# Kernel tuning notes

Hardware: AMD Instinct MI355X
Metric: run time of the kernel (lower is better)

The kernel has to match this reference:

```python
import jax, jax.numpy as jnp
import numpy as np
from jax import lax

C = 16  # channels

def _conv1x1(x, w, b):
    # 1x1x1 Conv3d == channel-mixing einsum. x: [B,C,T,H,W], w: [O,C], b: [O]
    return jnp.einsum('oc,bcthw->bothw', w, x) + b[None, :, None, None, None]

def _ffn(x, w1, b1, w2, b2):
    return _conv1x1(jnp.tanh(_conv1x1(x, w1, b1)), w2, b2)

def setup_inputs() -> dict:
    key = jax.random.key(0)
    ks = jax.random.split(key, 12)
    s = 0.1
    x = jax.random.normal(ks[0], (2, C, 31, 256, 256), dtype=jnp.float32)
    mk_w = lambda k: jax.random.normal(k, (C, C), dtype=jnp.float32) * s
    mk_b = lambda k: jax.random.normal(k, (C,), dtype=jnp.float32) * s
    return {
        'x': x,
        'wf1': mk_w(ks[1]), 'bf1': mk_b(ks[2]),
        'wf2': mk_w(ks[3]), 'bf2': mk_b(ks[4]),
        'ww1': mk_w(ks[5]), 'bw1': mk_b(ks[6]),
        'ww2': mk_w(ks[7]), 'bw2': mk_b(ks[8]),
        'wsca': mk_w(ks[9]), 'bsca': mk_b(ks[10]),
    }

def reference(x, wf1, bf1, wf2, bf2, ww1, bw1, ww2, bw2, wsca, bsca):
    # Gates from two 1x1-conv FFNs
    Z = jnp.tanh(_ffn(x, wf1, bf1, wf2, bf2))          # [B,C,T,H,W]
    Fg = jax.nn.sigmoid(_ffn(x, ww1, bw1, ww2, bw2))   # [B,C,T,H,W]
    # Linear recurrence over time dim: h_t = f_t * h_{t-1} + (1-f_t) * z_t, h_{-1}=0
    Zt = jnp.moveaxis(Z, 2, 0)   # [T,B,C,H,W]
    Ft = jnp.moveaxis(Fg, 2, 0)
    def step(h, zf):
        z, f = zf
        h = f * h + (1.0 - f) * z
        return h, h
    h0 = jnp.zeros_like(Zt[0])
    _, hs = lax.scan(step, h0, (Zt, Ft))
    out = jnp.moveaxis(hs, 0, 2)  # [B,C,T,H,W]
    # Simplified channel attention: global avg pool -> 1x1 conv -> sigmoid -> scale
    gap = jnp.mean(out, axis=(2, 3, 4), keepdims=True)  # [B,C,1,1,1]
    att = jax.nn.sigmoid(_conv1x1(gap, wsca, bsca))
    return att * out
```

## Files before the change

kernel.cpp:

```cpp
#include <hip/hip_runtime.h>
#include <hip/hip_bf16.h>

#define TDIM 31
#define TS   65536
#define CS   (TDIM * TS)
#define BS   (16 * CS)
#define NTOT (2 * BS)
#define K1_BLOCKS 8192
#define GAP_INV (1.0f / (31.0f * 65536.0f))

typedef __attribute__((ext_vector_type(8))) short short8v;
typedef __attribute__((ext_vector_type(4))) float f32x4;
typedef __attribute__((ext_vector_type(8))) unsigned short ushort8v;

__device__ __forceinline__ float frcp(float v){ return __builtin_amdgcn_rcpf(v); }
__device__ __forceinline__ float fexp2_(float v){ return __builtin_amdgcn_exp2f(v); }
__device__ __forceinline__ float ftanh(float x){ float e = fexp2_(x*2.8853900817779268f); return 1.0f - 2.0f*frcp(e+1.0f); }
__device__ __forceinline__ float fsigm(float x){ float e = fexp2_(x*-1.4426950408889634f); return frcp(1.0f+e); }
__device__ __forceinline__ unsigned rhu16(float x){ return (__float_as_uint(x) + 0x8000u) >> 16; }
__device__ __forceinline__ float bf2f(unsigned b){ return __uint_as_float(b << 16); }
__device__ __forceinline__ unsigned pkhi(unsigned u0, unsigned u1){ return __builtin_amdgcn_perm(u1, u0, 0x07060302u); }

template<bool BF16H>
__global__ __launch_bounds__(256, 4) void k1_fused(
    const float* __restrict__ x,
    const float* __restrict__ wf1, const float* __restrict__ bf1,
    const float* __restrict__ wf2, const float* __restrict__ bf2,
    const float* __restrict__ ww1, const float* __restrict__ bw1,
    const float* __restrict__ ww2, const float* __restrict__ bw2,
    float* __restrict__ out, unsigned short* __restrict__ hb,
    float* __restrict__ partials)
{
    __shared__ unsigned int sGate[TDIM * 256];

    const int tid  = threadIdx.x;
    const int lane = tid & 63;
    const int wv   = tid >> 6;
    const int col  = lane & 15;
    const int kg   = lane >> 4;
    const bool lok = (kg >= 2);
    const int blk  = blockIdx.x;
    const int b    = blk >> 12;
    const int p0   = (blk & 4095) << 4;

    short8v A1f, A2f, A1w, A2w, Af2, Aw2;
    {
        const int c0 = (kg & 1) * 8;
#pragma unroll
        for (int i = 0; i < 8; ++i) {
            const float w1 = wf1[col*16 + c0 + i];
            unsigned u1 = __float_as_uint(w1);
            float lo1 = w1 - __uint_as_float(u1 & 0xFFFF0000u);
            A1f[i] = (short)(u1 >> 16);
            A2f[i] = (short)(__float_as_uint(lo1) >> 16);
            const float w2 = ww1[col*16 + c0 + i];
            unsigned u2 = __float_as_uint(w2);
            float lo2 = w2 - __uint_as_float(u2 & 0xFFFF0000u);
            A1w[i] = (short)(u2 >> 16);
            A2w[i] = (short)(__float_as_uint(lo2) >> 16);
            const float v2f = wf2[col*16 + c0 + i];
            const float v2w = ww2[col*16 + c0 + i];
            Af2[i] = (kg < 2)  ? (short)rhu16(v2f) : (short)0;
            Aw2[i] = (kg >= 2) ? (short)rhu16(v2w) : (short)0;
        }
    }
    f32x4 b1fv, b1wv, b2fv, b2wv;
#pragma unroll
    for (int r = 0; r < 4; ++r) {
        b1fv[r] = bf1[kg*4+r]; b1wv[r] = bw1[kg*4+r];
        b2fv[r] = bf2[kg*4+r]; b2wv[r] = bw2[kg*4+r];
    }

    const int lsrc = col + ((kg & 1) << 5);

    auto process = [&](int u, const float* xv) {
        unsigned H[4], L[4];
#pragma unroll
        for (int j = 0; j < 4; ++j) {
            const unsigned u0 = __float_as_uint(xv[2*j]);
            const unsigned u1 = __float_as_uint(xv[2*j+1]);
            const float l0 = xv[2*j]   - __uint_as_float(u0 & 0xFFFF0000u);
            const float l1 = xv[2*j+1] - __uint_as_float(u1 & 0xFFFF0000u);
            H[j] = pkhi(u0, u1);
            L[j] = pkhi(__float_as_uint(l0), __float_as_uint(l1));
        }
        uint4 bxu;
        bxu.x = lok ? L[0] : H[0]; bxu.y = lok ? L[1] : H[1];
        bxu.z = lok ? L[2] : H[2]; bxu.w = lok ? L[3] : H[3];
        const short8v bx = __builtin_bit_cast(short8v, bxu);

        f32x4 accf = b1fv, accw = b1wv;
        accf = __builtin_amdgcn_mfma_f32_16x16x32_bf16(A1f, bx, accf, 0, 0, 0);
        accf = __builtin_amdgcn_mfma_f32_16x16x32_bf16(A2f, bx, accf, 0, 0, 0);
        accw = __builtin_amdgcn_mfma_f32_16x16x32_bf16(A1w, bx, accw, 0, 0, 0);
        accw = __builtin_amdgcn_mfma_f32_16x16x32_bf16(A2w, bx, accw, 0, 0, 0);

        const float a0 = ftanh(accf[0]), a1 = ftanh(accf[1]);
        const float a2 = ftanh(accf[2]), a3 = ftanh(accf[3]);
        const float w0 = ftanh(accw[0]), w1 = ftanh(accw[1]);
        const float w2 = ftanh(accw[2]), w3 = ftanh(accw[3]);
        const unsigned afP0 = (rhu16(a1) << 16) | rhu16(a0);
        const unsigned afP1 = (rhu16(a3) << 16) | rhu16(a2);
        const unsigned awP0 = (rhu16(w1) << 16) | rhu16(w0);
        const unsigned awP1 = (rhu16(w3) << 16) | rhu16(w2);

        const unsigned x0l = __shfl(afP0, lsrc, 64);
        const unsigned x1l = __shfl(afP1, lsrc, 64);
        const unsigned x0h = __shfl(afP0, lsrc + 16, 64);
        const unsigned x1h = __shfl(afP1, lsrc + 16, 64);
        const unsigned y0l = __shfl(awP0, lsrc, 64);
        const unsigned y1l = __shfl(awP1, lsrc, 64);
        const unsigned y0h = __shfl(awP0, lsrc + 16, 64);
        const unsigned y1h = __shfl(awP1, lsrc + 16, 64);
        uint4 b2u;
        b2u.x = lok ? y0l : x0l;
        b2u.y = lok ? y1l : x1l;
        b2u.z = lok ? y0h : x0h;
        b2u.w = lok ? y1h : x1h;
        const short8v b2 = __builtin_bit_cast(short8v, b2u);

        f32x4 acz = b2fv, acw = b2wv;
        acz = __builtin_amdgcn_mfma_f32_16x16x32_bf16(Af2, b2, acz, 0, 0, 0);
        acw = __builtin_amdgcn_mfma_f32_16x16x32_bf16(Aw2, b2, acw, 0, 0, 0);

#pragma unroll
        for (int r = 0; r < 4; ++r) {
            const float z = ftanh(acz[r]);
            const float f = fsigm(acw[r]);
            const int   zi = (int)__builtin_rintf(z * 32767.0f);
            const unsigned fu = (unsigned)(f * 65535.0f + 0.5f);
            const unsigned wd = ((unsigned)zi << 16) | (fu & 0xFFFFu);
            sGate[u*256 + r*64 + (kg>>1)*32 + (((r ^ kg) & 1) << 4)
                  + ((col + 4*r) & 15)] = wd;
        }
    };

    const unsigned xbase = (unsigned)b * BS + (unsigned)p0 + (unsigned)col
                         + (unsigned)((kg & 1) * 8) * CS;
#define LOADU(dst, u_) { const float* xp = x + (size_t)xbase + (size_t)(u_) * TS; \
    _Pragma("unroll") for (int i = 0; i < 8; ++i) (dst)[i] = xp[i * CS]; }

    float xs0[8], xs1[8], xs2[8], xs3[8];
    LOADU(xs0, wv)
    LOADU(xs1, wv + 4)
    LOADU(xs2, wv + 8)
#pragma unroll
    for (int k = 0; k < 8; ++k) {
        const int u  = wv + 4 * k;
        const int uf = u + 12;
        switch (k & 3) {
            case 0: if (uf < TDIM) LOADU(xs3, uf) if (u < TDIM) process(u, xs0); break;
            case 1: if (uf < TDIM) LOADU(xs0, uf) if (u < TDIM) process(u, xs1); break;
            case 2: if (uf < TDIM) LOADU(xs1, uf) if (u < TDIM) process(u, xs2); break;
            default:if (uf < TDIM) LOADU(xs2, uf) if (u < TDIM) process(u, xs3); break;
        }
    }
#undef LOADU
    __syncthreads();

    {
        const int c = tid >> 4, p = tid & 15;
        const unsigned base2 = (unsigned)((c & 3) * 64 + ((c >> 3) & 1) * 32
                             + (((c ^ (c >> 2)) & 1) << 4) + ((p + 4 * c) & 15));
        const unsigned obase = (unsigned)b * BS + (unsigned)c * CS
                             + (unsigned)p0 + (unsigned)p;
        float h = 0.f, s = 0.f;
#pragma unroll 1
        for (int t = 0; t < TDIM; ++t) {
            const unsigned wd = sGate[t * 256 + base2];
            const float z = (float)((int)wd >> 16) * (1.0f / 32767.0f);
            const float f = (float)(wd & 0xFFFFu) * (1.0f / 65535.0f);
            h = fmaf(f, h - z, z);
            s += h;
            if (BF16H) hb[obase + (unsigned)t * TS] = (unsigned short)rhu16(h);
            else       out[obase + (unsigned)t * TS] = h;
        }
#pragma unroll
        for (int off = 8; off; off >>= 1) s += __shfl_down(s, off, 16);
        if (p == 0) partials[blk * 16 + c] = s;
    }
}

__global__ __launch_bounds__(1024) void k2_attention(
    const float* __restrict__ partials, const float* __restrict__ wsca,
    const float* __restrict__ bsca, float* __restrict__ att)
{
    __shared__ float red[2][16][32];
    __shared__ float gap[2][16];
    const int tid = threadIdx.x;
    {
        const int b = tid >> 9, c = (tid >> 5) & 15, seg = tid & 31;
        float s = 0.f;
        const float* p = partials + (size_t)(b * 4096 + seg * 128) * 16 + c;
        for (int j = 0; j < 128; ++j) s += p[j * 16];
        red[b][c][seg] = s;
    }
    __syncthreads();
    if (tid < 32) {
        const int b = tid >> 4, c = tid & 15;
        float s = 0.f;
#pragma unroll
        for (int g = 0; g < 32; ++g) s += red[b][c][g];
        gap[b][c] = s * GAP_INV;
    }
    __syncthreads();
    if (tid < 32) {
        const int b = tid >> 4, o = tid & 15;
        float acc = bsca[o];
#pragma unroll
        for (int c = 0; c < 16; ++c) acc = fmaf(wsca[o*16 + c], gap[b][c], acc);
        att[b*16 + o] = fsigm(acc);
    }
}

__global__ __launch_bounds__(1024) void k3_scale_b(
    const unsigned short* __restrict__ hb, const float* __restrict__ att,
    float* __restrict__ out)
{
    const int bc = blockIdx.y;
    const float a = att[bc];
    const unsigned i = blockIdx.x * 1024 + threadIdx.x;
    const size_t base = (size_t)bc * CS;
    const ushort8v v = ((const ushort8v*)(hb + base))[i];
    float4 o1, o2;
    o1.x = bf2f(v[0])*a; o1.y = bf2f(v[1])*a; o1.z = bf2f(v[2])*a; o1.w = bf2f(v[3])*a;
    o2.x = bf2f(v[4])*a; o2.y = bf2f(v[5])*a; o2.z = bf2f(v[6])*a; o2.w = bf2f(v[7])*a;
    float4* op = (float4*)(out + base);
    op[i*2]     = o1;
    op[i*2 + 1] = o2;
}

__global__ __launch_bounds__(1024) void k3_scale_a(
    const float* __restrict__ att, float* __restrict__ out)
{
    const int bc = blockIdx.y;
    const float a = att[bc];
    const unsigned i = blockIdx.x * 1024 + threadIdx.x;
    float4* op = (float4*)(out + (size_t)bc * CS);
    float4 v1 = op[i*2], v2 = op[i*2 + 1];
    v1.x *= a; v1.y *= a; v1.z *= a; v1.w *= a;
    v2.x *= a; v2.y *= a; v2.z *= a; v2.w *= a;
    op[i*2] = v1; op[i*2 + 1] = v2;
}

extern "C" void kernel_launch(void* const* d_in, const int* in_sizes, int n_in,
                              void* d_out, int out_size, void* d_ws, size_t ws_size,
                              hipStream_t stream) {
    const float* x    = (const float*)d_in[0];
    const float* wf1  = (const float*)d_in[1];
    const float* bf1  = (const float*)d_in[2];
    const float* wf2  = (const float*)d_in[3];
    const float* bf2  = (const float*)d_in[4];
    const float* ww1  = (const float*)d_in[5];
    const float* bw1  = (const float*)d_in[6];
    const float* ww2  = (const float*)d_in[7];
    const float* bw2  = (const float*)d_in[8];
    const float* wsca = (const float*)d_in[9];
    const float* bsca = (const float*)d_in[10];
    float* out = (float*)d_out;

    const size_t hbBytes   = (size_t)NTOT * 2;
    const size_t partBytes = (size_t)K1_BLOCKS * 16 * 4;
    const bool bf16h = ws_size >= hbBytes + partBytes + 256;

    unsigned short* hb = (unsigned short*)d_ws;
    float* partials = bf16h ? (float*)((char*)d_ws + hbBytes) : (float*)d_ws;
    float* att = partials + K1_BLOCKS * 16;

    if (bf16h) {
        k1_fused<true><<<K1_BLOCKS, 256, 0, stream>>>(x, wf1, bf1, wf2, bf2,
            ww1, bw1, ww2, bw2, out, hb, partials);
        k2_attention<<<1, 1024, 0, stream>>>(partials, wsca, bsca, att);
        k3_scale_b<<<dim3(248, 32), 1024, 0, stream>>>(hb, att, out);
    } else {
        k1_fused<false><<<K1_BLOCKS, 256, 0, stream>>>(x, wf1, bf1, wf2, bf2,
            ww1, bw1, ww2, bw2, out, hb, partials);
        k2_attention<<<1, 1024, 0, stream>>>(partials, wsca, bsca, att);
        k3_scale_a<<<dim3(248, 32), 1024, 0, stream>>>(att, out);
    }
}
```

Baseline: 357.4 us.

## Split fused gate+scan kernel into separate gate and scan kernels via global buffer

Breaks the fused kernel in two. The first kernel computes the packed z/f gates with MFMA and writes them to global memory, using the output buffer as scratch. The second kernel runs the time recurrence per position, writes h and per-wave partial sums, and the attention reduction is re-indexed to match. This drops the LDS staging and the block-wide sync between the gate and scan phases, and frees occupancy from the shared-memory footprint. In exchange it adds a full extra global round trip of the gate tensor (about 260MB written and then read).

```diff
diff --git a/kernel.cpp b/kernel.cpp
--- a/kernel.cpp
+++ b/kernel.cpp
@@ -6,7 +6,6 @@
 #define CS   (TDIM * TS)
 #define BS   (16 * CS)
 #define NTOT (2 * BS)
-#define K1_BLOCKS 8192
 #define GAP_INV (1.0f / (31.0f * 65536.0f))
 
 typedef __attribute__((ext_vector_type(8))) short short8v;
@@ -21,18 +20,14 @@
 __device__ __forceinline__ float bf2f(unsigned b){ return __uint_as_float(b << 16); }
 __device__ __forceinline__ unsigned pkhi(unsigned u0, unsigned u1){ return __builtin_amdgcn_perm(u1, u0, 0x07060302u); }
 
-template<bool BF16H>
-__global__ __launch_bounds__(256, 4) void k1_fused(
+__global__ __launch_bounds__(256) void kA_gates(
     const float* __restrict__ x,
     const float* __restrict__ wf1, const float* __restrict__ bf1,
     const float* __restrict__ wf2, const float* __restrict__ bf2,
     const float* __restrict__ ww1, const float* __restrict__ bw1,
     const float* __restrict__ ww2, const float* __restrict__ bw2,
-    float* __restrict__ out, unsigned short* __restrict__ hb,
-    float* __restrict__ partials)
-{
-    __shared__ unsigned int sGate[TDIM * 256];
-
+    unsigned int* __restrict__ gates)
+{
     const int tid  = threadIdx.x;
     const int lane = tid & 63;
     const int wv   = tid >> 6;
@@ -72,6 +67,7 @@
     }
 
     const int lsrc = col + ((kg & 1) << 5);
+    const unsigned gbase = (unsigned)b * BS + (unsigned)p0 + (unsigned)col;
 
     auto process = [&](int u, const float* xv) {
         unsigned H[4], L[4];
@@ -130,8 +126,7 @@
             const int   zi = (int)__builtin_rintf(z * 32767.0f);
             const unsigned fu = (unsigned)(f * 65535.0f + 0.5f);
             const unsigned wd = ((unsigned)zi << 16) | (fu & 0xFFFFu);
-            sGate[u*256 + r*64 + (kg>>1)*32 + (((r ^ kg) & 1) << 4)
-                  + ((col + 4*r) & 15)] = wd;
+            gates[gbase + (unsigned)(kg*4 + r) * CS + (unsigned)u * TS] = wd;
         }
     };
 
@@ -156,59 +151,65 @@
         }
     }
 #undef LOADU
-    __syncthreads();
-
-    {
-        const int c = tid >> 4, p = tid & 15;
-        const unsigned base2 = (unsigned)((c & 3) * 64 + ((c >> 3) & 1) * 32
-                             + (((c ^ (c >> 2)) & 1) << 4) + ((p + 4 * c) & 15));
-        const unsigned obase = (unsigned)b * BS + (unsigned)c * CS
-                             + (unsigned)p0 + (unsigned)p;
-        float h = 0.f, s = 0.f;
-#pragma unroll 1
-        for (int t = 0; t < TDIM; ++t) {
-            const unsigned wd = sGate[t * 256 + base2];
-            const float z = (float)((int)wd >> 16) * (1.0f / 32767.0f);
-            const float f = (float)(wd & 0xFFFFu) * (1.0f / 65535.0f);
-            h = fmaf(f, h - z, z);
-            s += h;
-            if (BF16H) hb[obase + (unsigned)t * TS] = (unsigned short)rhu16(h);
-            else       out[obase + (unsigned)t * TS] = h;
-        }
-#pragma unroll
-        for (int off = 8; off; off >>= 1) s += __shfl_down(s, off, 16);
-        if (p == 0) partials[blk * 16 + c] = s;
-    }
+}
+
+template<bool BF16H>
+__global__ __launch_bounds__(256) void kB_scan(
+    unsigned int* __restrict__ gates,
+    unsigned short* __restrict__ hb,
+    float* __restrict__ partials)
+{
+    const int pos = blockIdx.x * 256 + threadIdx.x;
+    const int c   = blockIdx.y;
+    const int b   = blockIdx.z;
+    const unsigned base = (unsigned)b * BS + (unsigned)c * CS + (unsigned)pos;
+
+    float h = 0.f, s = 0.f;
+#pragma unroll
+    for (int t = 0; t < TDIM; ++t) {
+        const unsigned wd = gates[base + (unsigned)t * TS];
+        const float z = (float)((int)wd >> 16) * (1.0f / 32767.0f);
+        const float f = (float)(wd & 0xFFFFu) * (1.0f / 65535.0f);
+        h = fmaf(f, h - z, z);
+        s += h;
+        if (BF16H) hb[base + (unsigned)t * TS] = (unsigned short)rhu16(h);
+        else       ((float*)gates)[base + (unsigned)t * TS] = h;
+    }
+#pragma unroll
+    for (int off = 32; off; off >>= 1) s += __shfl_down(s, off, 64);
+    const int lane = threadIdx.x & 63, wvv = threadIdx.x >> 6;
+    if (lane == 0)
+        partials[(unsigned)(b * 16 + c) * 1024 + blockIdx.x * 4 + wvv] = s;
 }
 
 __global__ __launch_bounds__(1024) void k2_attention(
     const float* __restrict__ partials, const float* __restrict__ wsca,
     const float* __restrict__ bsca, float* __restrict__ att)
 {
-    __shared__ float red[2][16][32];
-    __shared__ float gap[2][16];
+    __shared__ float red[32][32];
+    __shared__ float gap[32];
     const int tid = threadIdx.x;
     {
-        const int b = tid >> 9, c = (tid >> 5) & 15, seg = tid & 31;
+        const int bc = tid >> 5, seg = tid & 31;
         float s = 0.f;
-        const float* p = partials + (size_t)(b * 4096 + seg * 128) * 16 + c;
-        for (int j = 0; j < 128; ++j) s += p[j * 16];
-        red[b][c][seg] = s;
+        const float* p = partials + (unsigned)bc * 1024 + seg * 32;
+#pragma unroll
+        for (int j = 0; j < 32; ++j) s += p[j];
+        red[bc][seg] = s;
     }
     __syncthreads();
     if (tid < 32) {
-        const int b = tid >> 4, c = tid & 15;
         float s = 0.f;
 #pragma unroll
-        for (int g = 0; g < 32; ++g) s += red[b][c][g];
-        gap[b][c] = s * GAP_INV;
+        for (int g = 0; g < 32; ++g) s += red[tid][g];
+        gap[tid] = s * GAP_INV;
     }
     __syncthreads();
     if (tid < 32) {
         const int b = tid >> 4, o = tid & 15;
         float acc = bsca[o];
 #pragma unroll
-        for (int c = 0; c < 16; ++c) acc = fmaf(wsca[o*16 + c], gap[b][c], acc);
+        for (int c = 0; c < 16; ++c) acc = fmaf(wsca[o*16 + c], gap[b*16 + c], acc);
         att[b*16 + o] = fsigm(acc);
     }
 }
@@ -260,21 +261,23 @@
     float* out = (float*)d_out;
 
     const size_t hbBytes   = (size_t)NTOT * 2;
-    const size_t partBytes = (size_t)K1_BLOCKS * 16 * 4;
+    const size_t partBytes = (size_t)32 * 1024 * 4;
     const bool bf16h = ws_size >= hbBytes + partBytes + 256;
 
+    unsigned int* gates = (unsigned int*)d_out;
     unsigned short* hb = (unsigned short*)d_ws;
     float* partials = bf16h ? (float*)((char*)d_ws + hbBytes) : (float*)d_ws;
-    float* att = partials + K1_BLOCKS * 16;
+    float* att = partials + 32 * 1024;
+
+    kA_gates<<<8192, 256, 0, stream>>>(
+        x, wf1, bf1, wf2, bf2, ww1, bw1, ww2, bw2, gates);
 
     if (bf16h) {
-        k1_fused<true><<<K1_BLOCKS, 256, 0, stream>>>(x, wf1, bf1, wf2, bf2,
-            ww1, bw1, ww2, bw2, out, hb, partials);
+        kB_scan<true><<<dim3(256, 16, 2), 256, 0, stream>>>(gates, hb, partials);
         k2_attention<<<1, 1024, 0, stream>>>(partials, wsca, bsca, att);
         k3_scale_b<<<dim3(248, 32), 1024, 0, stream>>>(hb, att, out);
     } else {
-        k1_fused<false><<<K1_BLOCKS, 256, 0, stream>>>(x, wf1, bf1, wf2, bf2,
-            ww1, bw1, ww2, bw2, out, hb, partials);
+        kB_scan<false><<<dim3(256, 16, 2), 256, 0, stream>>>(gates, hb, partials);
         k2_attention<<<1, 1024, 0, stream>>>(partials, wsca, bsca, att);
         k3_scale_a<<<dim3(248, 32), 1024, 0, stream>>>(att, out);
     }
```

Result: slower. 397.6 us (+11.2%).
